# Kernel optimization log

Hardware: AMD Instinct MI355X
Metric: run time of the kernel (lower is better)

## Reference

```python
import jax, jax.numpy as jnp
import numpy as np

B, NUM_OBJECTS, NUM_ATTRS, T = 8, 128, 4, 12
MAX_CONCEPTS, EMBED_DIM, IDENTITY_DIM, ATTENTION_DIM, HIDDEN_DIM = 2048, 128, 64, 64, 256
OP_MODE, OP_INSERT, OP_TRANSFER = 0, 1, 2


def setup_inputs() -> dict:
    key = jax.random.key(0)
    ks = jax.random.split(key, 24)
    def rn(k, shape, s=0.05):
        return s * jax.random.normal(k, shape, dtype=jnp.float32)
    return {
        'scene': jax.random.randint(ks[0], (B, NUM_OBJECTS, NUM_ATTRS), 0, MAX_CONCEPTS - 1),
        'program_op': jax.random.randint(ks[1], (B, T), 0, 3),
        'program_arg': jax.random.randint(ks[2], (B, T), 0, MAX_CONCEPTS),
        'attr_emb_in': rn(ks[3], (MAX_CONCEPTS, EMBED_DIM)),
        'attr_emb_out': rn(ks[4], (MAX_CONCEPTS, EMBED_DIM)),
        'attr_emb_id': rn(ks[5], (MAX_CONCEPTS, IDENTITY_DIM)),
        'concept_emb_in': rn(ks[6], (MAX_CONCEPTS, EMBED_DIM)),
        'concept_emb_out': rn(ks[7], (MAX_CONCEPTS, EMBED_DIM)),
        'concept_emb_id': rn(ks[8], (MAX_CONCEPTS, IDENTITY_DIM)),
        'embed_init': rn(ks[9], (EMBED_DIM,)),
        'identity_init': rn(ks[10], (IDENTITY_DIM,)),
        'attention_init': jnp.zeros((ATTENTION_DIM,), dtype=jnp.float32),
        'axon_w1': rn(ks[11], (HIDDEN_DIM, ATTENTION_DIM + IDENTITY_DIM)),
        'axon_b1': rn(ks[12], (HIDDEN_DIM,)),
        'axon_w2': rn(ks[13], (ATTENTION_DIM, HIDDEN_DIM)),
        'axon_b2': rn(ks[14], (ATTENTION_DIM,)),
        'meta_w1': rn(ks[15], (HIDDEN_DIM, EMBED_DIM + ATTENTION_DIM)),
        'meta_b1': rn(ks[16], (HIDDEN_DIM,)),
        'meta_w2': rn(ks[17], (ATTENTION_DIM, HIDDEN_DIM)),
        'meta_b2': rn(ks[18], (ATTENTION_DIM,)),
    }


def _mlp(x, w1, b1, w2, b2):
    # torch Linear convention: y = x @ W.T + b
    return jnp.maximum(x @ w1.T + b1, 0.0) @ w2.T + b2


def reference(scene, program_op, program_arg, attr_emb_in, attr_emb_out, attr_emb_id,
              concept_emb_in, concept_emb_out, concept_emb_id,
              embed_init, identity_init, attention_init,
              axon_w1, axon_b1, axon_w2, axon_b2,
              meta_w1, meta_b1, meta_w2, meta_b2):
    Bq, N, _ = scene.shape
    C = MAX_CONCEPTS + N  # dim_concept
    mask = (scene != -1).astype(jnp.float32)  # (B,N,A) non-background mask
    def embed_bg(E):
        return (E[scene + 1] * mask[..., None]).sum(2)  # (B,N,D)
    objects_in = embed_bg(attr_emb_in)
    objects_out = embed_bg(attr_emb_out)
    objects_id = embed_bg(attr_emb_id)

    rep = lambda w: jnp.broadcast_to(w[None], (Bq,) + w.shape)
    dendron = jnp.concatenate([rep(concept_emb_in), objects_in], 1)    # (B,C,E)
    axon = jnp.concatenate([rep(concept_emb_out), objects_out], 1)     # (B,C,E)
    identity = jnp.concatenate([rep(concept_emb_id), objects_id], 1)   # (B,C,Id)
    weight_matrix = jnp.einsum('bie,bje->bij', dendron, axon)           # (B,C,C)

    arguments = concept_emb_out[program_arg]                            # (B,T,E)
    is_mode = (program_op == OP_MODE).astype(jnp.float32)               # (B,T)
    is_insert = (program_op == OP_INSERT).astype(jnp.float32)
    is_transfer = (program_op == OP_TRANSFER).astype(jnp.float32)

    meta0 = jnp.broadcast_to(attention_init[None], (Bq, ATTENTION_DIM))
    att0 = jnp.broadcast_to(attention_init[None, None], (Bq, C, ATTENTION_DIM))

    def step(carry, xs):
        meta, attention = carry
        arg_i, m, ins, tr = xs  # (B,E), (B,), (B,), (B,)
        new_meta = _mlp(jnp.concatenate([meta, arg_i], 1), meta_w1, meta_b1, meta_w2, meta_b2)
        meta = m[:, None] * new_meta + (1.0 - m[:, None]) * meta
        # (arguments * axon).mean over embed dim -> (B,C)
        proj = jnp.einsum('be,bce->bc', arg_i, axon) / EMBED_DIM
        attention_insert = meta[:, None, :] * proj[:, :, None]          # (B,C,A)
        attended_weight = weight_matrix * attention.mean(2)[:, None, :] # (B,C,C)
        ia = jnp.concatenate([identity, attention], 2)                  # (B,C,Id+A)
        # (attended_weight[:,:,:,None] * ia[:,None]).mean(2) == matmul / C
        gathered = jnp.einsum('bij,bjd->bid', attended_weight, ia) / C  # (B,C,Id+A)
        attention_transfer = _mlp(gathered, axon_w1, axon_b1, axon_w2, axon_b2) + gathered[..., IDENTITY_DIM:]
        attention = attention + ins[:, None, None] * attention_insert + tr[:, None, None] * attention_transfer
        attention = jnp.clip(jnp.where(attention >= 0, attention, 0.01 * attention), -1.0, 2.0)
        return (meta, attention), (attention, attention_insert, attention_transfer)

    xs = (jnp.swapaxes(arguments, 0, 1), is_mode.T, is_insert.T, is_transfer.T)
    (meta, attention), (att_hist, ins_hist, trans_hist) = jax.lax.scan(step, (meta0, att0), xs)
    output_softmax = jax.nn.log_softmax(attention.mean(2), axis=1)  # (B,C)
    return (output_softmax, att_hist, ins_hist, trans_hist)
```

## Files before the change

### kernel.cpp

```cpp
#include <hip/hip_runtime.h>

#define B 8
#define NOBJ 128
#define NATTR 4
#define T 12
#define MC 2048
#define E 128
#define IDD 64
#define AD 64
#define HD 256
#define C 2176

typedef short s16x8 __attribute__((ext_vector_type(8)));
typedef float f32x4 __attribute__((ext_vector_type(4)));

__device__ inline unsigned short f2b(float f) {
  union { float f; unsigned u; } v; v.f = f;
  unsigned r = v.u + 0x7FFFu + ((v.u >> 16) & 1u);
  return (unsigned short)(r >> 16);
}
__device__ inline float b2f(unsigned short u) {
  union { unsigned u; float f; } v; v.u = ((unsigned)u) << 16;
  return v.f;
}

__device__ __forceinline__ void st_coh_u64(unsigned long long* p, unsigned long long v) {
  __hip_atomic_store(p, v, __ATOMIC_RELAXED, __HIP_MEMORY_SCOPE_AGENT);
}
__device__ __forceinline__ void st_coh_u32(unsigned* p, unsigned v) {
  __hip_atomic_store(p, v, __ATOMIC_RELAXED, __HIP_MEMORY_SCOPE_AGENT);
}
__device__ __forceinline__ unsigned ld_coh_u32(const unsigned* p) {
  return __hip_atomic_load(p, __ATOMIC_RELAXED, __HIP_MEMORY_SCOPE_AGENT);
}

__device__ __forceinline__ int gidx(int r, int c) {
  return r * 128 + ((((c >> 3) ^ (r & 15)) << 3) | (c & 7));
}
__device__ __forceinline__ int hidx(int r, int c) {
  return r * 256 + ((((c >> 3) ^ (r & 15)) << 3) | (c & 7));
}
__device__ __forceinline__ int mtidx(int r, int c) {
  return r * 128 + ((((c >> 3) ^ (r & 15)) << 3) | (c & 7));
}

__global__ __launch_bounds__(256) void k_setup(
    const int* __restrict__ scene,
    const float* __restrict__ aein, const float* __restrict__ aeout,
    const float* __restrict__ aeid,
    const float* __restrict__ cein, const float* __restrict__ ceout,
    const float* __restrict__ ceid,
    const float* __restrict__ att_init,
    const int* __restrict__ prog_op, const int* __restrict__ prog_arg,
    const float* __restrict__ aw1, const float* __restrict__ aw2,
    const float* __restrict__ mw1, const float* __restrict__ mb1,
    const float* __restrict__ mw2, const float* __restrict__ mb2,
    unsigned short* __restrict__ dendron_bf,
    unsigned short* __restrict__ w1_bf, unsigned short* __restrict__ w2_bf,
    unsigned short* __restrict__ axonT, unsigned short* __restrict__ idT_g,
    unsigned short* __restrict__ siaT, float* __restrict__ att_g,
    float* __restrict__ meta_all, float* __restrict__ proj_all,
    unsigned* __restrict__ flags) {
  int blk = blockIdx.x;
  int tid = threadIdx.x;
  if (blk < 4352) {
    int gid = blk * 2 + (tid >> 7);
    int e = tid & 127;
    int b = gid / C, j = gid % C;
    float din;
    if (j < MC) {
      din = cein[j * E + e];
    } else {
      int obj = j - MC;
      float sIn = 0.f;
      for (int a = 0; a < NATTR; a++) {
        int s = scene[(b * NOBJ + obj) * NATTR + a];
        float m = (s != -1) ? 1.f : 0.f;
        sIn += aein[(s + 1) * E + e] * m;
      }
      din = sIn;
    }
    dendron_bf[(size_t)gid * E + e] = f2b(din);
  } else if (blk < 4544) {
    int i = (blk - 4352) * 256 + tid;
    if (i < HD * E)  w1_bf[i] = f2b(aw1[i]);
    if (i < AD * HD) w2_bf[i] = f2b(aw2[i]);
    float* mw1T = meta_all + (size_t)T * B * AD;
    (void)mw1T;
  } else if (blk < 4816) {
    int sb = blk - 4544;
    int b = sb / 34, jc = sb % 34;
    int j0 = jc * 64;
    __shared__ float ax[64][129];
    __shared__ float idb[64][65];
    int lane = tid & 63, lr = lane & 15;
    float s = att_init[lane];
    s += __shfl_xor(s, 1, 64);  s += __shfl_xor(s, 2, 64);
    s += __shfl_xor(s, 4, 64);  s += __shfl_xor(s, 8, 64);
    s += __shfl_xor(s, 16, 64); s += __shfl_xor(s, 32, 64);
    float am0 = s * (1.f / AD);
    for (int i = tid; i < 64 * 128; i += 256) {
      int j = i >> 7, e = i & 127;
      int jg = j0 + j;
      float v;
      if (jg < MC) v = ceout[jg * E + e];
      else {
        int obj = jg - MC;
        v = 0.f;
        for (int a = 0; a < NATTR; a++) {
          int sc = scene[(b * NOBJ + obj) * NATTR + a];
          float m = (sc != -1) ? 1.f : 0.f;
          v += aeout[(sc + 1) * E + e] * m;
        }
      }
      ax[j][e] = v;
    }
    for (int i = tid; i < 64 * 64; i += 256) {
      int j = i >> 6, d = i & 63;
      int jg = j0 + j;
      float v;
      if (jg < MC) v = ceid[jg * IDD + d];
      else {
        int obj = jg - MC;
        v = 0.f;
        for (int a = 0; a < NATTR; a++) {
          int sc = scene[(b * NOBJ + obj) * NATTR + a];
          float m = (sc != -1) ? 1.f : 0.f;
          v += aeid[(sc + 1) * IDD + d] * m;
        }
      }
      idb[j][d] = v;
    }
    __syncthreads();
    for (int i = tid; i < 128 * 64; i += 256) {
      int e = i >> 6, jj = i & 63;
      axonT[(size_t)(b * E + e) * C + j0 + jj] = f2b(ax[jj][e]);
    }
    for (int i = tid; i < 64 * 64; i += 256) {
      int d = i >> 6, jj = i & 63;
      idT_g[(size_t)(b * 64 + d) * C + j0 + jj] = f2b(idb[jj][d]);
      siaT[(size_t)(b * 128 + d) * C + j0 + jj] = f2b(idb[jj][d] * am0);
      siaT[(size_t)(b * 128 + 64 + d) * C + j0 + jj] = f2b(att_init[d] * am0);
    }
    {
      float* ag = att_g + (size_t)sb * 4096 + tid * 16;
      #pragma unroll
      for (int n = 0; n < 4; n++) {
        float v0 = att_init[n * 16 + lr];
        #pragma unroll
        for (int v = 0; v < 4; v++) ag[n * 4 + v] = v0;
      }
    }
  } else if (blk < 4824) {
    int b = blk - 4816;
    __shared__ float x[192];
    __shared__ float h[HD];
    __shared__ float meta[AD];
    if (tid < AD) meta[tid] = att_init[tid];
    __syncthreads();
    for (int t = 0; t < T; t++) {
      int arg = prog_arg[b * T + t];
      if (tid < AD) x[tid] = meta[tid];
      else if (tid < 192) x[tid] = ceout[arg * E + (tid - 64)];
      __syncthreads();
      float s = mb1[tid];
      for (int c = 0; c < 192; c++) s += x[c] * mw1[tid * 192 + c];
      h[tid] = fmaxf(s, 0.f);
      __syncthreads();
      if (tid < AD) {
        float o = mb2[tid];
        for (int k = 0; k < HD; k++) o += h[k] * mw2[tid * HD + k];
        float m = (prog_op[b * T + t] == 0) ? 1.f : 0.f;
        float nm = m * o + (1.f - m) * meta[tid];
        meta[tid] = nm;
        meta_all[(t * B + b) * AD + tid] = nm;
      }
      __syncthreads();
    }
  } else if (blk < 9176) {
    int gid = (blk - 4824) * 4 + (tid >> 6);
    int lane = tid & 63;
    int b = gid / C, i = gid % C;
    float a0, a1;
    if (i < MC) {
      a0 = ceout[i * E + lane];
      a1 = ceout[i * E + 64 + lane];
    } else {
      int obj = i - MC;
      a0 = 0.f; a1 = 0.f;
      for (int a = 0; a < NATTR; a++) {
        int sc = scene[(b * NOBJ + obj) * NATTR + a];
        float m = (sc != -1) ? 1.f : 0.f;
        a0 += aeout[(sc + 1) * E + lane] * m;
        a1 += aeout[(sc + 1) * E + 64 + lane] * m;
      }
    }
    for (int t = 0; t < T; t++) {
      int arg = prog_arg[b * T + t];
      float p = a0 * ceout[arg * E + lane] + a1 * ceout[arg * E + 64 + lane];
      for (int off2 = 1; off2 < 64; off2 <<= 1) p += __shfl_xor(p, off2, 64);
      if (lane == 0) proj_all[(size_t)(t * B + b) * C + i] = p * (1.f / E);
    }
  } else {
    if (tid < 256) flags[tid] = 0u;
  }
}

__global__ __launch_bounds__(256) void k_step(
    int t,
    const unsigned short* __restrict__ dendron_bf,
    const unsigned short* __restrict__ axonT,
    const unsigned short* __restrict__ idT_g,
    const unsigned short* __restrict__ siaT_in,
    const unsigned short* __restrict__ w1_bf, const float* __restrict__ b1g,
    const unsigned short* __restrict__ w2_bf, const float* __restrict__ b2g,
    const float* __restrict__ proj_all, const float* __restrict__ meta_all,
    const int* __restrict__ prog_op,
    unsigned long long* __restrict__ Mt64,
    float* __restrict__ att_g, unsigned short* __restrict__ siaT_out,
    float* __restrict__ rowmean,
    float* __restrict__ att_hist, float* __restrict__ ins_hist,
    float* __restrict__ trans_hist,
    unsigned* __restrict__ mflag) {
  const int blk = blockIdx.x;
  const int b = blk / 34, ch = blk % 34, j0 = ch * 64;
  const int tid = threadIdx.x;
  const int w = tid >> 6, lane = tid & 63, lr = lane & 15, lg = lane >> 4;

  __shared__ unsigned short smem[24576];
  __shared__ float am_l[64];
  unsigned short* g_l = smem;
  unsigned short* mt  = smem + 8192;
  unsigned short* h_l = smem + 8192;
  float* mred = (float*)smem;

  const f32x4 z = {0.f, 0.f, 0.f, 0.f};
  const unsigned ph = (unsigned)(t + 1);

  float att[4][4];
  {
    const f32x4* ag = (const f32x4*)(att_g + (size_t)blk * 4096 + tid * 16);
    #pragma unroll
    for (int n = 0; n < 4; n++) {
      f32x4 v4 = ag[n];
      #pragma unroll
      for (int v = 0; v < 4; v++) att[n][v] = v4[v];
    }
  }

  if (ch < 16) {
    int d0 = (ch >> 2) * 32, e0 = (ch & 3) * 32;
    const unsigned short* ap0 = siaT_in + (size_t)(b * 128 + d0 + lr) * C + w * 544 + lg * 8;
    const unsigned short* ap1 = ap0 + (size_t)16 * C;
    const unsigned short* bp0 = axonT + (size_t)(b * E + e0 + lr) * C + w * 544 + lg * 8;
    const unsigned short* bp1 = bp0 + (size_t)16 * C;
    f32x4 a00 = z, a01 = z, a10 = z, a11 = z;
    #pragma unroll 4
    for (int kk = 0; kk < 17; kk++) {
      int k0 = kk * 32;
      s16x8 A0 = *(const s16x8*)(ap0 + k0);
      s16x8 A1 = *(const s16x8*)(ap1 + k0);
      s16x8 B0 = *(const s16x8*)(bp0 + k0);
      s16x8 B1 = *(const s16x8*)(bp1 + k0);
      a00 = __builtin_amdgcn_mfma_f32_16x16x32_bf16(A0, B0, a00, 0, 0, 0);
      a01 = __builtin_amdgcn_mfma_f32_16x16x32_bf16(A0, B1, a01, 0, 0, 0);
      a10 = __builtin_amdgcn_mfma_f32_16x16x32_bf16(A1, B0, a10, 0, 0, 0);
      a11 = __builtin_amdgcn_mfma_f32_16x16x32_bf16(A1, B1, a11, 0, 0, 0);
    }
    #pragma unroll
    for (int v = 0; v < 4; v++) {
      mred[(w * 32 + lg * 4 + v) * 33 + lr]           = a00[v];
      mred[(w * 32 + lg * 4 + v) * 33 + 16 + lr]      = a01[v];
      mred[(w * 32 + 16 + lg * 4 + v) * 33 + lr]      = a10[v];
      mred[(w * 32 + 16 + lg * 4 + v) * 33 + 16 + lr] = a11[v];
    }
    __syncthreads();
    {
      int r = tid >> 3, c = (tid & 7) * 4;
      float s0 = 0.f, s1 = 0.f, s2 = 0.f, s3 = 0.f;
      #pragma unroll
      for (int w4 = 0; w4 < 4; w4++) {
        const float* p = &mred[(w4 * 32 + r) * 33 + c];
        s0 += p[0]; s1 += p[1]; s2 += p[2]; s3 += p[3];
      }
      unsigned long long pk = (unsigned long long)f2b(s0)
                            | ((unsigned long long)f2b(s1) << 16)
                            | ((unsigned long long)f2b(s2) << 32)
                            | ((unsigned long long)f2b(s3) << 48);
      st_coh_u64(Mt64 + (((size_t)(b * 128 + d0 + r) * 128) + e0 + c) / 4, pk);
    }
    asm volatile("s_waitcnt vmcnt(0)" ::: "memory");
    __syncthreads();
    if (tid == 0) st_coh_u32(mflag + b * 16 + ch, ph);
  }
  if (tid < 16) {
    while (ld_coh_u32(mflag + b * 16 + tid) < ph) __builtin_amdgcn_s_sleep(1);
  }
  __syncthreads();
  {
    const unsigned long long* mtp = Mt64 + (size_t)b * 4096;
    #pragma unroll
    for (int k = 0; k < 16; k++) {
      int idx = tid + k * 256;
      unsigned long long v = mtp[idx];
      int r = idx >> 5, c4 = (idx & 31) * 4;
      *(unsigned long long*)&mt[mtidx(r, c4)] = v;
    }
  }
  __syncthreads();
  {
    s16x8 afr[4];
    #pragma unroll
    for (int ke = 0; ke < 4; ke++)
      afr[ke] = *(const s16x8*)(dendron_bf + (size_t)(b * C + j0 + w * 16 + lr) * E + ke * 32 + lg * 8);
    #pragma unroll
    for (int n = 0; n < 8; n++) {
      f32x4 acc = z;
      #pragma unroll
      for (int ke = 0; ke < 4; ke++) {
        s16x8 bf = *(const s16x8*)&mt[mtidx(n * 16 + lr, ke * 32 + lg * 8)];
        acc = __builtin_amdgcn_mfma_f32_16x16x32_bf16(afr[ke], bf, acc, 0, 0, 0);
      }
      #pragma unroll
      for (int v = 0; v < 4; v++)
        g_l[gidx(w * 16 + lg * 4 + v, n * 16 + lr)] = f2b(acc[v] * (1.f / C));
    }
  }
  __syncthreads();
  {
    s16x8 gf[4];
    #pragma unroll
    for (int kd = 0; kd < 4; kd++)
      gf[kd] = *(const s16x8*)&g_l[gidx(w * 16 + lr, kd * 32 + lg * 8)];
    #pragma unroll
    for (int n = 0; n < 16; n++) {
      f32x4 acc = z;
      #pragma unroll
      for (int kd = 0; kd < 4; kd++) {
        s16x8 bf = *(const s16x8*)(w1_bf + (size_t)(n * 16 + lr) * E + kd * 32 + lg * 8);
        acc = __builtin_amdgcn_mfma_f32_16x16x32_bf16(gf[kd], bf, acc, 0, 0, 0);
      }
      float b1v = b1g[n * 16 + lr];
      #pragma unroll
      for (int v = 0; v < 4; v++)
        h_l[hidx(w * 16 + lg * 4 + v, n * 16 + lr)] = f2b(fmaxf(acc[v] + b1v, 0.f));
    }
  }
  __syncthreads();
  {
    s16x8 hf[8];
    #pragma unroll
    for (int kk = 0; kk < 8; kk++)
      hf[kk] = *(const s16x8*)&h_l[hidx(w * 16 + lr, kk * 32 + lg * 8)];
    int op = prog_op[b * T + t];
    float insF = (op == 1) ? 1.f : 0.f, trF = (op == 2) ? 1.f : 0.f;
    float projv[4];
    #pragma unroll
    for (int v = 0; v < 4; v++)
      projv[v] = proj_all[(size_t)(t * B + b) * C + j0 + w * 16 + lg * 4 + v];
    #pragma unroll
    for (int n = 0; n < 4; n++) {
      f32x4 acc = z;
      #pragma unroll
      for (int kk = 0; kk < 8; kk++) {
        s16x8 bf = *(const s16x8*)(w2_bf + (size_t)(n * 16 + lr) * HD + kk * 32 + lg * 8);
        acc = __builtin_amdgcn_mfma_f32_16x16x32_bf16(hf[kk], bf, acc, 0, 0, 0);
      }
      int a = n * 16 + lr;
      float b2v = b2g[a];
      float meta_a = meta_all[(size_t)(t * B + b) * AD + a];
      #pragma unroll
      for (int v = 0; v < 4; v++) {
        int row = lg * 4 + v;
        int i = j0 + w * 16 + row;
        float transfer = acc[v] + b2v + b2f(g_l[gidx(w * 16 + row, 64 + a)]);
        float insert = meta_a * projv[v];
        float attv = att[n][v] + insF * insert + trF * transfer;
        attv = (attv >= 0.f) ? attv : 0.01f * attv;
        attv = fminf(fmaxf(attv, -1.f), 2.f);
        att[n][v] = attv;
        size_t hi = (((size_t)t * B + b) * C + i) * AD + a;
        __builtin_nontemporal_store(attv, att_hist + hi);
        __builtin_nontemporal_store(insert, ins_hist + hi);
        __builtin_nontemporal_store(transfer, trans_hist + hi);
      }
    }
  }
  float amr[4];
  {
    float s[4];
    #pragma unroll
    for (int v = 0; v < 4; v++) s[v] = att[0][v] + att[1][v] + att[2][v] + att[3][v];
    #pragma unroll
    for (int v = 0; v < 4; v++) {
      s[v] += __shfl_xor(s[v], 1, 64);
      s[v] += __shfl_xor(s[v], 2, 64);
      s[v] += __shfl_xor(s[v], 4, 64);
      s[v] += __shfl_xor(s[v], 8, 64);
      amr[v] = s[v] * (1.f / AD);
    }
    if (lr == 0) {
      #pragma unroll
      for (int v = 0; v < 4; v++) {
        am_l[w * 16 + lg * 4 + v] = amr[v];
        rowmean[(size_t)b * C + j0 + w * 16 + lg * 4 + v] = amr[v];
      }
    }
  }
  {
    f32x4* ag = (f32x4*)(att_g + (size_t)blk * 4096 + tid * 16);
    #pragma unroll
    for (int n = 0; n < 4; n++) {
      f32x4 v4;
      #pragma unroll
      for (int v = 0; v < 4; v++) v4[v] = att[n][v];
      ag[n] = v4;
      unsigned long long pk = 0;
      #pragma unroll
      for (int v = 0; v < 4; v++)
        pk |= (unsigned long long)f2b(att[n][v] * amr[v]) << (16 * v);
      *(unsigned long long*)(siaT_out + (size_t)(b * 128 + 64 + n * 16 + lr) * C + j0 + w * 16 + lg * 4) = pk;
    }
  }
  __syncthreads();
  #pragma unroll
  for (int k2 = 0; k2 < 2; k2++) {
    int idx = tid + k2 * 256;
    int d = idx >> 3, part = idx & 7;
    int j = part * 8;
    s16x8 iv = *(const s16x8*)(idT_g + (size_t)(b * 64 + d) * C + j0 + j);
    s16x8 ov;
    #pragma unroll
    for (int m = 0; m < 8; m++)
      ov[m] = (short)f2b(b2f((unsigned short)iv[m]) * am_l[j + m]);
    *(s16x8*)(siaT_out + (size_t)(b * 128 + d) * C + j0 + j) = ov;
  }
}

__global__ void k_softmax(const float* __restrict__ rowmean, float* __restrict__ out) {
  int b = blockIdx.x;
  __shared__ float am[C];
  __shared__ float red[256];
  int tid = threadIdx.x;
  for (int i = tid; i < C; i += 256) am[i] = rowmean[(size_t)b * C + i];
  __syncthreads();
  float mx = -1e30f;
  for (int i = tid; i < C; i += 256) mx = fmaxf(mx, am[i]);
  red[tid] = mx; __syncthreads();
  for (int s = 128; s > 0; s >>= 1) { if (tid < s) red[tid] = fmaxf(red[tid], red[tid + s]); __syncthreads(); }
  mx = red[0]; __syncthreads();
  float sm = 0.f;
  for (int i = tid; i < C; i += 256) sm += expf(am[i] - mx);
  red[tid] = sm; __syncthreads();
  for (int s = 128; s > 0; s >>= 1) { if (tid < s) red[tid] += red[tid + s]; __syncthreads(); }
  float lse = logf(red[0]) + mx;
  for (int i = tid; i < C; i += 256) out[(size_t)b * C + i] = am[i] - lse;
}

extern "C" void kernel_launch(void* const* d_in, const int* in_sizes, int n_in,
                              void* d_out, int out_size, void* d_ws, size_t ws_size,
                              hipStream_t stream) {
  const int* scene     = (const int*)d_in[0];
  const int* prog_op   = (const int*)d_in[1];
  const int* prog_arg  = (const int*)d_in[2];
  const float* aein    = (const float*)d_in[3];
  const float* aeout   = (const float*)d_in[4];
  const float* aeid    = (const float*)d_in[5];
  const float* cein    = (const float*)d_in[6];
  const float* ceout   = (const float*)d_in[7];
  const float* ceid    = (const float*)d_in[8];
  const float* att_init = (const float*)d_in[11];
  const float* aw1 = (const float*)d_in[12];
  const float* ab1 = (const float*)d_in[13];
  const float* aw2 = (const float*)d_in[14];
  const float* ab2 = (const float*)d_in[15];
  const float* mw1 = (const float*)d_in[16];
  const float* mb1 = (const float*)d_in[17];
  const float* mw2 = (const float*)d_in[18];
  const float* mb2 = (const float*)d_in[19];

  char* ws = (char*)d_ws;
  size_t off = 0;
  auto carve = [&](size_t bytes) { char* p = ws + off; off += (bytes + 255) & ~(size_t)255; return p; };
  float* proj_all  = (float*)carve((size_t)T * B * C * 4);
  float* meta_all  = (float*)carve((size_t)T * B * AD * 4 + 4096);
  float* rowmean   = (float*)carve((size_t)B * C * 4);
  float* att_g     = (float*)carve((size_t)272 * 4096 * 4);
  unsigned short* dendron_bf = (unsigned short*)carve((size_t)B * C * E * 2);
  unsigned short* axonT      = (unsigned short*)carve((size_t)B * E * C * 2);
  unsigned short* idT_g      = (unsigned short*)carve((size_t)B * 64 * C * 2);
  unsigned short* siaT       = (unsigned short*)carve((size_t)B * 128 * C * 2);
  unsigned long long* Mt64   = (unsigned long long*)carve((size_t)B * 4096 * 8);
  unsigned short* w1_bf      = (unsigned short*)carve((size_t)HD * E * 2);
  unsigned short* w2_bf      = (unsigned short*)carve((size_t)AD * HD * 2);
  unsigned*       mflag      = (unsigned*)carve(1024);

  float* out_sm     = (float*)d_out;
  float* att_hist   = out_sm + B * C;
  float* ins_hist   = att_hist + (size_t)T * B * C * AD;
  float* trans_hist = ins_hist + (size_t)T * B * C * AD;

  k_setup<<<dim3(9177), dim3(256), 0, stream>>>(scene, aein, aeout, aeid, cein, ceout, ceid,
                                                att_init, prog_op, prog_arg,
                                                aw1, aw2, mw1, mb1, mw2, mb2,
                                                dendron_bf, w1_bf, w2_bf,
                                                axonT, idT_g, siaT, att_g,
                                                meta_all, proj_all, mflag);
  for (int t = 0; t < T; t++) {
    k_step<<<dim3(272), dim3(256), 0, stream>>>(t, dendron_bf, axonT, idT_g, siaT,
                                                w1_bf, ab1, w2_bf, ab2,
                                                proj_all, meta_all, prog_op,
                                                Mt64, att_g, siaT, rowmean,
                                                att_hist, ins_hist, trans_hist, mflag);
  }
  k_softmax<<<dim3(B), dim3(256), 0, stream>>>(rowmean, out_sm);
}
```

Measured before the change: 683.8 us.

## Split setup kernel, compute projections from staged tiles, fuse softmax into last step

The monolithic setup kernel is split in two. The second part computes the per-step projections from the already-staged axon tile in shared memory instead of running thousands of wave-reduction blocks, and the meta MLP now reads pre-transposed weights so its loads coalesce. The final step kernel skips its unneeded att_g/siaT writes, publishes row means with coherent stores, and block 0 of each batch spins on flags to compute the log-softmax, which removes the separate softmax launch. This adds an extra launch and a spin-wait that relies on all blocks being co-resident.

```diff
diff --git a/kernel.cpp b/kernel.cpp
--- a/kernel.cpp
+++ b/kernel.cpp
@@ -30,6 +30,10 @@
 __device__ __forceinline__ void st_coh_u32(unsigned* p, unsigned v) {
   __hip_atomic_store(p, v, __ATOMIC_RELAXED, __HIP_MEMORY_SCOPE_AGENT);
 }
+__device__ __forceinline__ void st_coh_f32(float* p, float v) {
+  union { float f; unsigned u; } c; c.f = v;
+  __hip_atomic_store((unsigned*)p, c.u, __ATOMIC_RELAXED, __HIP_MEMORY_SCOPE_AGENT);
+}
 __device__ __forceinline__ unsigned ld_coh_u32(const unsigned* p) {
   return __hip_atomic_load(p, __ATOMIC_RELAXED, __HIP_MEMORY_SCOPE_AGENT);
 }
@@ -44,22 +48,15 @@
   return r * 128 + ((((c >> 3) ^ (r & 15)) << 3) | (c & 7));
 }
 
-__global__ __launch_bounds__(256) void k_setup(
+__global__ __launch_bounds__(256) void k_setupA(
     const int* __restrict__ scene,
-    const float* __restrict__ aein, const float* __restrict__ aeout,
-    const float* __restrict__ aeid,
-    const float* __restrict__ cein, const float* __restrict__ ceout,
-    const float* __restrict__ ceid,
-    const float* __restrict__ att_init,
-    const int* __restrict__ prog_op, const int* __restrict__ prog_arg,
+    const float* __restrict__ aein,
+    const float* __restrict__ cein,
     const float* __restrict__ aw1, const float* __restrict__ aw2,
-    const float* __restrict__ mw1, const float* __restrict__ mb1,
-    const float* __restrict__ mw2, const float* __restrict__ mb2,
+    const float* __restrict__ mw1, const float* __restrict__ mw2,
     unsigned short* __restrict__ dendron_bf,
     unsigned short* __restrict__ w1_bf, unsigned short* __restrict__ w2_bf,
-    unsigned short* __restrict__ axonT, unsigned short* __restrict__ idT_g,
-    unsigned short* __restrict__ siaT, float* __restrict__ att_g,
-    float* __restrict__ meta_all, float* __restrict__ proj_all,
+    float* __restrict__ mw1T, float* __restrict__ mw2T,
     unsigned* __restrict__ flags) {
   int blk = blockIdx.x;
   int tid = threadIdx.x;
@@ -85,14 +82,33 @@
     int i = (blk - 4352) * 256 + tid;
     if (i < HD * E)  w1_bf[i] = f2b(aw1[i]);
     if (i < AD * HD) w2_bf[i] = f2b(aw2[i]);
-    float* mw1T = meta_all + (size_t)T * B * AD;
-    (void)mw1T;
-  } else if (blk < 4816) {
-    int sb = blk - 4544;
-    int b = sb / 34, jc = sb % 34;
+    if (i < 192 * HD) { int c = i / HD, k = i % HD; mw1T[c * HD + k] = mw1[k * 192 + c]; }
+    if (i < HD * AD)  { int k = i / AD, a = i % AD; mw2T[k * AD + a] = mw2[a * HD + k]; }
+  } else {
+    for (int i = tid; i < 512; i += 256) flags[i] = 0u;
+  }
+}
+
+__global__ __launch_bounds__(256) void k_setupB(
+    const int* __restrict__ scene,
+    const float* __restrict__ aeout, const float* __restrict__ aeid,
+    const float* __restrict__ ceout, const float* __restrict__ ceid,
+    const float* __restrict__ att_init,
+    const int* __restrict__ prog_op, const int* __restrict__ prog_arg,
+    const float* __restrict__ mw1T, const float* __restrict__ mb1,
+    const float* __restrict__ mw2T, const float* __restrict__ mb2,
+    unsigned short* __restrict__ axonT, unsigned short* __restrict__ idT_g,
+    unsigned short* __restrict__ siaT, float* __restrict__ att_g,
+    float* __restrict__ meta_all, float* __restrict__ proj_all) {
+  int blk = blockIdx.x;
+  int tid = threadIdx.x;
+  __shared__ float sbuf[13952];
+  if (blk < 272) {
+    int b = blk / 34, jc = blk % 34;
     int j0 = jc * 64;
-    __shared__ float ax[64][129];
-    __shared__ float idb[64][65];
+    float* ax   = sbuf;
+    float* idb  = sbuf + 64 * 129;
+    float* argL = idb + 64 * 65;
     int lane = tid & 63, lr = lane & 15;
     float s = att_init[lane];
     s += __shfl_xor(s, 1, 64);  s += __shfl_xor(s, 2, 64);
@@ -113,7 +129,7 @@
           v += aeout[(sc + 1) * E + e] * m;
         }
       }
-      ax[j][e] = v;
+      ax[j * 129 + e] = v;
     }
     for (int i = tid; i < 64 * 64; i += 256) {
       int j = i >> 6, d = i & 63;
@@ -129,21 +145,26 @@
           v += aeid[(sc + 1) * IDD + d] * m;
         }
       }
-      idb[j][d] = v;
+      idb[j * 65 + d] = v;
+    }
+    for (int i = tid; i < T * 128; i += 256) {
+      int t = i >> 7, e = i & 127;
+      int arg = prog_arg[b * T + t];
+      argL[t * 128 + e] = ceout[arg * E + e];
     }
     __syncthreads();
     for (int i = tid; i < 128 * 64; i += 256) {
       int e = i >> 6, jj = i & 63;
-      axonT[(size_t)(b * E + e) * C + j0 + jj] = f2b(ax[jj][e]);
+      axonT[(size_t)(b * E + e) * C + j0 + jj] = f2b(ax[jj * 129 + e]);
     }
     for (int i = tid; i < 64 * 64; i += 256) {
       int d = i >> 6, jj = i & 63;
-      idT_g[(size_t)(b * 64 + d) * C + j0 + jj] = f2b(idb[jj][d]);
-      siaT[(size_t)(b * 128 + d) * C + j0 + jj] = f2b(idb[jj][d] * am0);
+      idT_g[(size_t)(b * 64 + d) * C + j0 + jj] = f2b(idb[jj * 65 + d]);
+      siaT[(size_t)(b * 128 + d) * C + j0 + jj] = f2b(idb[jj * 65 + d] * am0);
       siaT[(size_t)(b * 128 + 64 + d) * C + j0 + jj] = f2b(att_init[d] * am0);
     }
     {
-      float* ag = att_g + (size_t)sb * 4096 + tid * 16;
+      float* ag = att_g + (size_t)blk * 4096 + tid * 16;
       #pragma unroll
       for (int n = 0; n < 4; n++) {
         float v0 = att_init[n * 16 + lr];
@@ -151,11 +172,24 @@
         for (int v = 0; v < 4; v++) ag[n * 4 + v] = v0;
       }
     }
-  } else if (blk < 4824) {
-    int b = blk - 4816;
-    __shared__ float x[192];
-    __shared__ float h[HD];
-    __shared__ float meta[AD];
+    {
+      int jj = tid & 63, tq = tid >> 6;
+      #pragma unroll
+      for (int sI = 0; sI < 3; sI++) {
+        int t = tq + 4 * sI;
+        const float* ar = argL + t * 128;
+        const float* axr = ax + jj * 129;
+        float acc = 0.f;
+        #pragma unroll 8
+        for (int e = 0; e < 128; e++) acc += axr[e] * ar[e];
+        proj_all[((size_t)t * B + b) * C + j0 + jj] = acc * (1.f / E);
+      }
+    }
+  } else {
+    int b = blk - 272;
+    float* x = sbuf;
+    float* h = sbuf + 192;
+    float* meta = h + 256;
     if (tid < AD) meta[tid] = att_init[tid];
     __syncthreads();
     for (int t = 0; t < T; t++) {
@@ -164,12 +198,12 @@
       else if (tid < 192) x[tid] = ceout[arg * E + (tid - 64)];
       __syncthreads();
       float s = mb1[tid];
-      for (int c = 0; c < 192; c++) s += x[c] * mw1[tid * 192 + c];
+      for (int c = 0; c < 192; c++) s += x[c] * mw1T[c * HD + tid];
       h[tid] = fmaxf(s, 0.f);
       __syncthreads();
       if (tid < AD) {
         float o = mb2[tid];
-        for (int k = 0; k < HD; k++) o += h[k] * mw2[tid * HD + k];
+        for (int k = 0; k < HD; k++) o += h[k] * mw2T[k * AD + tid];
         float m = (prog_op[b * T + t] == 0) ? 1.f : 0.f;
         float nm = m * o + (1.f - m) * meta[tid];
         meta[tid] = nm;
@@ -177,32 +211,6 @@
       }
       __syncthreads();
     }
-  } else if (blk < 9176) {
-    int gid = (blk - 4824) * 4 + (tid >> 6);
-    int lane = tid & 63;
-    int b = gid / C, i = gid % C;
-    float a0, a1;
-    if (i < MC) {
-      a0 = ceout[i * E + lane];
-      a1 = ceout[i * E + 64 + lane];
-    } else {
-      int obj = i - MC;
-      a0 = 0.f; a1 = 0.f;
-      for (int a = 0; a < NATTR; a++) {
-        int sc = scene[(b * NOBJ + obj) * NATTR + a];
-        float m = (sc != -1) ? 1.f : 0.f;
-        a0 += aeout[(sc + 1) * E + lane] * m;
-        a1 += aeout[(sc + 1) * E + 64 + lane] * m;
-      }
-    }
-    for (int t = 0; t < T; t++) {
-      int arg = prog_arg[b * T + t];
-      float p = a0 * ceout[arg * E + lane] + a1 * ceout[arg * E + 64 + lane];
-      for (int off2 = 1; off2 < 64; off2 <<= 1) p += __shfl_xor(p, off2, 64);
-      if (lane == 0) proj_all[(size_t)(t * B + b) * C + i] = p * (1.f / E);
-    }
-  } else {
-    if (tid < 256) flags[tid] = 0u;
   }
 }
 
@@ -218,10 +226,10 @@
     const int* __restrict__ prog_op,
     unsigned long long* __restrict__ Mt64,
     float* __restrict__ att_g, unsigned short* __restrict__ siaT_out,
-    float* __restrict__ rowmean,
+    float* __restrict__ rowmean, float* __restrict__ out,
     float* __restrict__ att_hist, float* __restrict__ ins_hist,
     float* __restrict__ trans_hist,
-    unsigned* __restrict__ mflag) {
+    unsigned* __restrict__ mflag, unsigned* __restrict__ sflag) {
   const int blk = blockIdx.x;
   const int b = blk / 34, ch = blk % 34, j0 = ch * 64;
   const int tid = threadIdx.x;
@@ -229,6 +237,7 @@
 
   __shared__ unsigned short smem[24576];
   __shared__ float am_l[64];
+  __shared__ float red[256];
   unsigned short* g_l = smem;
   unsigned short* mt  = smem + 8192;
   unsigned short* h_l = smem + 8192;
@@ -401,60 +410,68 @@
     }
     if (lr == 0) {
       #pragma unroll
-      for (int v = 0; v < 4; v++) {
-        am_l[w * 16 + lg * 4 + v] = amr[v];
-        rowmean[(size_t)b * C + j0 + w * 16 + lg * 4 + v] = amr[v];
-      }
-    }
-  }
-  {
-    f32x4* ag = (f32x4*)(att_g + (size_t)blk * 4096 + tid * 16);
-    #pragma unroll
-    for (int n = 0; n < 4; n++) {
-      f32x4 v4;
-      #pragma unroll
-      for (int v = 0; v < 4; v++) v4[v] = att[n][v];
-      ag[n] = v4;
-      unsigned long long pk = 0;
+      for (int v = 0; v < 4; v++) am_l[w * 16 + lg * 4 + v] = amr[v];
+    }
+  }
+  if (t < T - 1) {
+    {
+      f32x4* ag = (f32x4*)(att_g + (size_t)blk * 4096 + tid * 16);
+      #pragma unroll
+      for (int n = 0; n < 4; n++) {
+        f32x4 v4;
+        #pragma unroll
+        for (int v = 0; v < 4; v++) v4[v] = att[n][v];
+        ag[n] = v4;
+        unsigned long long pk = 0;
+        #pragma unroll
+        for (int v = 0; v < 4; v++)
+          pk |= (unsigned long long)f2b(att[n][v] * amr[v]) << (16 * v);
+        *(unsigned long long*)(siaT_out + (size_t)(b * 128 + 64 + n * 16 + lr) * C + j0 + w * 16 + lg * 4) = pk;
+      }
+    }
+    __syncthreads();
+    #pragma unroll
+    for (int k2 = 0; k2 < 2; k2++) {
+      int idx = tid + k2 * 256;
+      int d = idx >> 3, part = idx & 7;
+      int j = part * 8;
+      s16x8 iv = *(const s16x8*)(idT_g + (size_t)(b * 64 + d) * C + j0 + j);
+      s16x8 ov;
+      #pragma unroll
+      for (int m = 0; m < 8; m++)
+        ov[m] = (short)f2b(b2f((unsigned short)iv[m]) * am_l[j + m]);
+      *(s16x8*)(siaT_out + (size_t)(b * 128 + d) * C + j0 + j) = ov;
+    }
+  } else {
+    if (lr == 0) {
       #pragma unroll
       for (int v = 0; v < 4; v++)
-        pk |= (unsigned long long)f2b(att[n][v] * amr[v]) << (16 * v);
-      *(unsigned long long*)(siaT_out + (size_t)(b * 128 + 64 + n * 16 + lr) * C + j0 + w * 16 + lg * 4) = pk;
-    }
-  }
-  __syncthreads();
-  #pragma unroll
-  for (int k2 = 0; k2 < 2; k2++) {
-    int idx = tid + k2 * 256;
-    int d = idx >> 3, part = idx & 7;
-    int j = part * 8;
-    s16x8 iv = *(const s16x8*)(idT_g + (size_t)(b * 64 + d) * C + j0 + j);
-    s16x8 ov;
-    #pragma unroll
-    for (int m = 0; m < 8; m++)
-      ov[m] = (short)f2b(b2f((unsigned short)iv[m]) * am_l[j + m]);
-    *(s16x8*)(siaT_out + (size_t)(b * 128 + d) * C + j0 + j) = ov;
-  }
-}
-
-__global__ void k_softmax(const float* __restrict__ rowmean, float* __restrict__ out) {
-  int b = blockIdx.x;
-  __shared__ float am[C];
-  __shared__ float red[256];
-  int tid = threadIdx.x;
-  for (int i = tid; i < C; i += 256) am[i] = rowmean[(size_t)b * C + i];
-  __syncthreads();
-  float mx = -1e30f;
-  for (int i = tid; i < C; i += 256) mx = fmaxf(mx, am[i]);
-  red[tid] = mx; __syncthreads();
-  for (int s = 128; s > 0; s >>= 1) { if (tid < s) red[tid] = fmaxf(red[tid], red[tid + s]); __syncthreads(); }
-  mx = red[0]; __syncthreads();
-  float sm = 0.f;
-  for (int i = tid; i < C; i += 256) sm += expf(am[i] - mx);
-  red[tid] = sm; __syncthreads();
-  for (int s = 128; s > 0; s >>= 1) { if (tid < s) red[tid] += red[tid + s]; __syncthreads(); }
-  float lse = logf(red[0]) + mx;
-  for (int i = tid; i < C; i += 256) out[(size_t)b * C + i] = am[i] - lse;
+        st_coh_f32(rowmean + (size_t)b * C + j0 + w * 16 + lg * 4 + v, amr[v]);
+    }
+    asm volatile("s_waitcnt vmcnt(0)" ::: "memory");
+    __syncthreads();
+    if (tid == 0) st_coh_u32(sflag + b * 34 + ch, 1u);
+    if (ch == 0) {
+      if (tid < 34) {
+        while (ld_coh_u32(sflag + b * 34 + tid) < 1u) __builtin_amdgcn_s_sleep(1);
+      }
+      __syncthreads();
+      float* am = (float*)smem;
+      for (int i = tid; i < C; i += 256) am[i] = rowmean[(size_t)b * C + i];
+      __syncthreads();
+      float mx = -1e30f;
+      for (int i = tid; i < C; i += 256) mx = fmaxf(mx, am[i]);
+      red[tid] = mx; __syncthreads();
+      for (int s2 = 128; s2 > 0; s2 >>= 1) { if (tid < s2) red[tid] = fmaxf(red[tid], red[tid + s2]); __syncthreads(); }
+      mx = red[0]; __syncthreads();
+      float sm = 0.f;
+      for (int i = tid; i < C; i += 256) sm += expf(am[i] - mx);
+      red[tid] = sm; __syncthreads();
+      for (int s2 = 128; s2 > 0; s2 >>= 1) { if (tid < s2) red[tid] += red[tid + s2]; __syncthreads(); }
+      float lse = logf(red[0]) + mx;
+      for (int i = tid; i < C; i += 256) out[(size_t)b * C + i] = am[i] - lse;
+    }
+  }
 }
 
 extern "C" void kernel_launch(void* const* d_in, const int* in_sizes, int n_in,
@@ -483,7 +500,9 @@
   size_t off = 0;
   auto carve = [&](size_t bytes) { char* p = ws + off; off += (bytes + 255) & ~(size_t)255; return p; };
   float* proj_all  = (float*)carve((size_t)T * B * C * 4);
-  float* meta_all  = (float*)carve((size_t)T * B * AD * 4 + 4096);
+  float* meta_all  = (float*)carve((size_t)T * B * AD * 4);
+  float* mw1T      = (float*)carve((size_t)192 * HD * 4);
+  float* mw2T      = (float*)carve((size_t)HD * AD * 4);
   float* rowmean   = (float*)carve((size_t)B * C * 4);
   float* att_g     = (float*)carve((size_t)272 * 4096 * 4);
   unsigned short* dendron_bf = (unsigned short*)carve((size_t)B * C * E * 2);
@@ -493,25 +512,27 @@
   unsigned long long* Mt64   = (unsigned long long*)carve((size_t)B * 4096 * 8);
   unsigned short* w1_bf      = (unsigned short*)carve((size_t)HD * E * 2);
   unsigned short* w2_bf      = (unsigned short*)carve((size_t)AD * HD * 2);
-  unsigned*       mflag      = (unsigned*)carve(1024);
+  unsigned*       flags      = (unsigned*)carve(2048);
+  unsigned*       mflag = flags;
+  unsigned*       sflag = flags + 128;
 
   float* out_sm     = (float*)d_out;
   float* att_hist   = out_sm + B * C;
   float* ins_hist   = att_hist + (size_t)T * B * C * AD;
   float* trans_hist = ins_hist + (size_t)T * B * C * AD;
 
-  k_setup<<<dim3(9177), dim3(256), 0, stream>>>(scene, aein, aeout, aeid, cein, ceout, ceid,
-                                                att_init, prog_op, prog_arg,
-                                                aw1, aw2, mw1, mb1, mw2, mb2,
-                                                dendron_bf, w1_bf, w2_bf,
+  k_setupA<<<dim3(4545), dim3(256), 0, stream>>>(scene, aein, cein, aw1, aw2, mw1, mw2,
+                                                 dendron_bf, w1_bf, w2_bf, mw1T, mw2T, flags);
+  k_setupB<<<dim3(280), dim3(256), 0, stream>>>(scene, aeout, aeid, ceout, ceid, att_init,
+                                                prog_op, prog_arg, mw1T, mb1, mw2T, mb2,
                                                 axonT, idT_g, siaT, att_g,
-                                                meta_all, proj_all, mflag);
+                                                meta_all, proj_all);
   for (int t = 0; t < T; t++) {
     k_step<<<dim3(272), dim3(256), 0, stream>>>(t, dendron_bf, axonT, idT_g, siaT,
                                                 w1_bf, ab1, w2_bf, ab2,
                                                 proj_all, meta_all, prog_op,
-                                                Mt64, att_g, siaT, rowmean,
-                                                att_hist, ins_hist, trans_hist, mflag);
-  }
-  k_softmax<<<dim3(B), dim3(256), 0, stream>>>(rowmean, out_sm);
-}
+                                                Mt64, att_g, siaT, rowmean, out_sm,
+                                                att_hist, ins_hist, trans_hist,
+                                                mflag, sflag);
+  }
+}
```

Result: faster. 648.1 us, median of 2 (-5.2%).
